# Kernel tuning notes

Hardware: AMD Instinct MI355X
Metric: run time of the kernel (lower is better)

Reference implementation:

```python
import jax, jax.numpy as jnp
import numpy as np

N = 100000   # num_nodes
D = 128      # hidden_dim
E = 640000   # num_edges


def setup_inputs() -> dict:
    key = jax.random.key(0)
    k0, k1, k2, k3 = jax.random.split(key, 4)
    node_features = jax.random.normal(k0, (N, D), dtype=jnp.float32) * 0.02
    # GCNConv linear weights (glorot-style scale), bias initialized to zero
    scale = 1.0 / np.sqrt(D)
    W1 = jax.random.normal(k1, (D, D), dtype=jnp.float32) * scale
    b1 = jnp.zeros((D,), dtype=jnp.float32)
    W2 = jax.random.normal(k2, (D, D), dtype=jnp.float32) * scale
    b2 = jnp.zeros((D,), dtype=jnp.float32)
    edge_index = jax.random.randint(k3, (2, E), 0, N, dtype=jnp.int32)
    return {"node_features": node_features, "W1": W1, "b1": b1,
            "W2": W2, "b2": b2, "edge_index": edge_index}


def gcn_layer(x, W, b, row, col):
    # PyG GCNConv: linear (no bias) -> symmetric norm deg^-1/2 -> scatter-add -> +bias
    x = x @ W.T                                   # [N, D]
    ones = jnp.ones(row.shape, dtype=x.dtype)
    deg = jax.ops.segment_sum(ones, col, num_segments=N)   # in-degree incl. self-loops
    dis = jnp.where(deg > 0, jax.lax.rsqrt(deg), 0.0)       # deg_inv_sqrt, inf -> 0
    norm = dis[row] * dis[col]                    # [E_tot]
    msgs = norm[:, None] * x[row]                 # gather + scale, [E_tot, D]
    out = jax.ops.segment_sum(msgs, col, num_segments=N)    # scatter-aggregate
    return out + b


def reference(node_features, W1, b1, W2, b2, edge_index):
    # add self-loops once (GCNConv does this per call; same result since graph is static)
    loops = jnp.arange(N, dtype=edge_index.dtype)
    row = jnp.concatenate([edge_index[0], loops])
    col = jnp.concatenate([edge_index[1], loops])
    x = jax.nn.relu(gcn_layer(node_features, W1, b1, row, col))
    x = jax.nn.relu(gcn_layer(x, W2, b2, row, col))
    return x
```

## Files before the change

kernel.cpp:

```cpp
#include <hip/hip_runtime.h>

#define DD 128

typedef short bf16x8 __attribute__((ext_vector_type(8)));
typedef float f32x4 __attribute__((ext_vector_type(4)));

__device__ __forceinline__ unsigned short f2bf(float f) {
    unsigned int u = __builtin_bit_cast(unsigned int, f);
    u += 0x7fffu + ((u >> 16) & 1u);
    return (unsigned short)(u >> 16);
}
__device__ __forceinline__ float bflo(unsigned int u) { return __builtin_bit_cast(float, u << 16); }
__device__ __forceinline__ float bfhi(unsigned int u) { return __builtin_bit_cast(float, u & 0xffff0000u); }

__global__ __launch_bounds__(512) void k_count(const int* __restrict__ col,
                                               int* __restrict__ cnt, int E) {
    int e = blockIdx.x * 512 + threadIdx.x;
    if (e < E) atomicAdd(&cnt[col[e]], 1);
}

__global__ __launch_bounds__(256) void k_part(const int* __restrict__ cnt,
                                              int* __restrict__ part, int n) {
    __shared__ int s[256];
    int t = threadIdx.x;
    int i = blockIdx.x * 256 + t;
    s[t] = (i < n) ? cnt[i] : 0;
    __syncthreads();
    for (int off = 128; off > 0; off >>= 1) {
        if (t < off) s[t] += s[t + off];
        __syncthreads();
    }
    if (t == 0) part[blockIdx.x] = s[0];
}

__global__ __launch_bounds__(1024) void k_scanpart(int* __restrict__ part, int nblk) {
    __shared__ int s[1024];
    int t = threadIdx.x;
    int v = (t < nblk) ? part[t] : 0;
    s[t] = v;
    __syncthreads();
    for (int off = 1; off < 1024; off <<= 1) {
        int u = (t >= off) ? s[t - off] : 0;
        __syncthreads();
        s[t] += u;
        __syncthreads();
    }
    if (t < nblk) part[t] = s[t] - v;
}

__global__ __launch_bounds__(256) void k_apply(const int* __restrict__ cnt,
                                               const int* __restrict__ part,
                                               int* __restrict__ rowptr,
                                               int* __restrict__ cursor,
                                               float* __restrict__ dis, int n) {
    __shared__ int s[256];
    int t = threadIdx.x;
    int i = blockIdx.x * 256 + t;
    int c = (i < n) ? cnt[i] : 0;
    s[t] = c;
    __syncthreads();
    for (int off = 1; off < 256; off <<= 1) {
        int u = (t >= off) ? s[t - off] : 0;
        __syncthreads();
        s[t] += u;
        __syncthreads();
    }
    int base = part[blockIdx.x] + s[t] - c;
    if (i < n) {
        rowptr[i] = base;
        cursor[i] = base;
        dis[i] = rsqrtf((float)c + 1.0f);
        if (i == n - 1) rowptr[n] = base + c;
    }
}

#define TILES 2
template <bool INBF16, bool FUSE_PERM>
__global__ __launch_bounds__(512) void k_gemm_mfma(const void* __restrict__ Xv,
                                                   const float* __restrict__ W,
                                                   unsigned short* __restrict__ Y,
                                                   int nrows, int gemm_blocks,
                                                   const int* __restrict__ erow,
                                                   const int* __restrict__ ecol,
                                                   int* __restrict__ cursor,
                                                   int* __restrict__ srow, int E) {
    __shared__ unsigned short Ws[128 * 128];
    const int t = threadIdx.x;

    if (FUSE_PERM && blockIdx.x >= gemm_blocks) {
        int e = (blockIdx.x - gemm_blocks) * 512 + t;
        if (e < E) {
            int p = atomicAdd(&cursor[ecol[e]], 1);
            srow[p] = erow[e];
        }
        return;
    }

    #pragma unroll
    for (int i = 0; i < 4; ++i) {
        int g  = i * 512 + t;
        int wr = g >> 4, ch = g & 15;
        const float* src = W + wr * 128 + ch * 8;
        float4 f0 = *(const float4*)src;
        float4 f1 = *(const float4*)(src + 4);
        unsigned short u[8] = { f2bf(f0.x), f2bf(f0.y), f2bf(f0.z), f2bf(f0.w),
                                f2bf(f1.x), f2bf(f1.y), f2bf(f1.z), f2bf(f1.w) };
        int dst = wr * 128 + ((ch ^ (wr & 15)) << 3);
        *(uint4*)&Ws[dst] = *(const uint4*)u;
    }
    __syncthreads();

    const int wid  = t >> 6;
    const int lane = t & 63;
    const int lr   = lane & 15;
    const int lk   = lane >> 4;

    #pragma unroll
    for (int tile = 0; tile < TILES; ++tile) {
        const long base = ((long)blockIdx.x * TILES + tile) * 128;
        long arow = base + wid * 16 + lr;
        bool rowok = arow < nrows;
        if (!rowok) arow = nrows - 1;

        f32x4 acc[8] = {};

        #pragma unroll
        for (int kc = 0; kc < 4; ++kc) {
            bf16x8 af;
            if (INBF16) {
                const unsigned short* ap = (const unsigned short*)Xv + arow * 128 + kc * 32 + lk * 8;
                af = *(const bf16x8*)ap;
            } else {
                const float* ap = (const float*)Xv + arow * 128 + kc * 32 + lk * 8;
                float4 a0 = *(const float4*)ap;
                float4 a1 = *(const float4*)(ap + 4);
                af[0] = (short)f2bf(a0.x); af[1] = (short)f2bf(a0.y);
                af[2] = (short)f2bf(a0.z); af[3] = (short)f2bf(a0.w);
                af[4] = (short)f2bf(a1.x); af[5] = (short)f2bf(a1.y);
                af[6] = (short)f2bf(a1.z); af[7] = (short)f2bf(a1.w);
            }
            #pragma unroll
            for (int jt = 0; jt < 8; ++jt) {
                int j  = jt * 16 + lr;
                int ch = (kc * 4 + lk) ^ lr;
                const bf16x8* bp = (const bf16x8*)&Ws[j * 128 + (ch << 3)];
                acc[jt] = __builtin_amdgcn_mfma_f32_16x16x32_bf16(*bp, af, acc[jt], 0, 0, 0);
            }
        }

        if (rowok) {
            unsigned short* yp = Y + arow * 128 + lk * 4;
            #pragma unroll
            for (int jt = 0; jt < 8; ++jt) {
                unsigned int d0 = (unsigned int)f2bf(acc[jt][0]) | ((unsigned int)f2bf(acc[jt][1]) << 16);
                unsigned int d1 = (unsigned int)f2bf(acc[jt][2]) | ((unsigned int)f2bf(acc[jt][3]) << 16);
                uint2 u; u.x = d0; u.y = d1;
                *(uint2*)(yp + jt * 16) = u;
            }
        }
    }
}

__device__ __forceinline__ void fma8(float* acc, float nm, uint4 q) {
    acc[0] += nm * bflo(q.x); acc[1] += nm * bfhi(q.x);
    acc[2] += nm * bflo(q.y); acc[3] += nm * bfhi(q.y);
    acc[4] += nm * bflo(q.z); acc[5] += nm * bfhi(q.z);
    acc[6] += nm * bflo(q.w); acc[7] += nm * bfhi(q.w);
}

template <bool OUTBF16>
__global__ __launch_bounds__(256) void k_agg(const int* __restrict__ rowptr,
                                             const int* __restrict__ srow,
                                             const float* __restrict__ dis,
                                             const unsigned short* __restrict__ xw,
                                             const float* __restrict__ b,
                                             void* __restrict__ outv, int n) {
    int v = blockIdx.x * 16 + (threadIdx.x >> 4);
    if (v >= n) return;
    int c = (threadIdx.x & 15) * 8;

    float dv = dis[v], s = dv * dv;
    float acc[8] = {};
    fma8(acc, s, *(const uint4*)(xw + (long)v * 128 + c));

    int e0 = rowptr[v], e1 = rowptr[v + 1];
    int e = e0;
    for (; e + 4 <= e1; e += 4) {
        int   r1 = srow[e],     r2 = srow[e + 1];
        int   r3 = srow[e + 2], r4 = srow[e + 3];
        float n1 = dis[r1] * dv, n2 = dis[r2] * dv;
        float n3 = dis[r3] * dv, n4 = dis[r4] * dv;
        uint4 q1 = *(const uint4*)(xw + (long)r1 * 128 + c);
        uint4 q2 = *(const uint4*)(xw + (long)r2 * 128 + c);
        uint4 q3 = *(const uint4*)(xw + (long)r3 * 128 + c);
        uint4 q4 = *(const uint4*)(xw + (long)r4 * 128 + c);
        fma8(acc, n1, q1);
        fma8(acc, n2, q2);
        fma8(acc, n3, q3);
        fma8(acc, n4, q4);
    }
    for (; e < e1; ++e) {
        int   r1 = srow[e];
        float n1 = dis[r1] * dv;
        fma8(acc, n1, *(const uint4*)(xw + (long)r1 * 128 + c));
    }

    float4 b0 = *(const float4*)(b + c);
    float4 b1 = *(const float4*)(b + c + 4);
    float o[8];
    o[0] = fmaxf(acc[0] + b0.x, 0.0f); o[1] = fmaxf(acc[1] + b0.y, 0.0f);
    o[2] = fmaxf(acc[2] + b0.z, 0.0f); o[3] = fmaxf(acc[3] + b0.w, 0.0f);
    o[4] = fmaxf(acc[4] + b1.x, 0.0f); o[5] = fmaxf(acc[5] + b1.y, 0.0f);
    o[6] = fmaxf(acc[6] + b1.z, 0.0f); o[7] = fmaxf(acc[7] + b1.w, 0.0f);

    if (OUTBF16) {
        unsigned int pk[4];
        pk[0] = (unsigned int)f2bf(o[0]) | ((unsigned int)f2bf(o[1]) << 16);
        pk[1] = (unsigned int)f2bf(o[2]) | ((unsigned int)f2bf(o[3]) << 16);
        pk[2] = (unsigned int)f2bf(o[4]) | ((unsigned int)f2bf(o[5]) << 16);
        pk[3] = (unsigned int)f2bf(o[6]) | ((unsigned int)f2bf(o[7]) << 16);
        *(uint4*)((unsigned short*)outv + (long)v * 128 + c) = *(const uint4*)pk;
    } else {
        float* op = (float*)outv + (long)v * 128 + c;
        *(float4*)op       = make_float4(o[0], o[1], o[2], o[3]);
        *(float4*)(op + 4) = make_float4(o[4], o[5], o[6], o[7]);
    }
}

extern "C" void kernel_launch(void* const* d_in, const int* in_sizes, int n_in,
                              void* d_out, int out_size, void* d_ws, size_t ws_size,
                              hipStream_t stream) {
    const float* X  = (const float*)d_in[0];
    const float* W1 = (const float*)d_in[1];
    const float* b1 = (const float*)d_in[2];
    const float* W2 = (const float*)d_in[3];
    const float* b2 = (const float*)d_in[4];
    const int*   ei = (const int*)d_in[5];
    const int N = in_sizes[0] / DD;
    const int E = in_sizes[5] / 2;
    const int* row = ei;
    const int* col = ei + E;

    char* p = (char*)d_ws;
    auto carve = [&](size_t bytes) { char* q = p; p += (bytes + 255) & ~(size_t)255; return q; };
    int*            cnt    = (int*)           carve((size_t)N * 4);
    int*            rowptr = (int*)           carve((size_t)(N + 1) * 4);
    int*            cursor = (int*)           carve((size_t)N * 4);
    int*            part   = (int*)           carve(1024 * 4);
    int*            srow   = (int*)           carve((size_t)E * 4);
    float*          dis    = (float*)         carve((size_t)N * 4);
    unsigned short* xw     = (unsigned short*)carve((size_t)N * DD * 2);
    unsigned short* h1     = (unsigned short*)d_out;

    const int NBLK = (N + 255) / 256;
    const int gemm_grid  = (N + 128 * TILES - 1) / (128 * TILES);
    const int edge_grid  = (E + 511) / 512;
    const int agg_grid   = (N + 15) / 16;

    hipMemsetAsync(cnt, 0, (size_t)N * 4, stream);
    k_count<<<edge_grid, 512, 0, stream>>>(col, cnt, E);
    k_part<<<NBLK, 256, 0, stream>>>(cnt, part, N);
    k_scanpart<<<1, 1024, 0, stream>>>(part, NBLK);
    k_apply<<<NBLK, 256, 0, stream>>>(cnt, part, rowptr, cursor, dis, N);

    k_gemm_mfma<false, true><<<gemm_grid + edge_grid, 512, 0, stream>>>(
        X, W1, xw, N, gemm_grid, row, col, cursor, srow, E);

    k_agg<true><<<agg_grid, 256, 0, stream>>>(rowptr, srow, dis, xw, b1, h1, N);

    k_gemm_mfma<true, false><<<gemm_grid, 512, 0, stream>>>(
        h1, W2, xw, N, gemm_grid, nullptr, nullptr, nullptr, nullptr, 0);
    k_agg<false><<<agg_grid, 256, 0, stream>>>(rowptr, srow, dis, xw, b2, d_out, N);
}
```

Baseline: 183.6 us.

## Fuse layer-1 aggregation with layer-2 GEMM through shared memory

Measured after the change: 194.1 us. +5.7%, slower.

```diff
diff --git a/kernel.cpp b/kernel.cpp
--- a/kernel.cpp
+++ b/kernel.cpp
@@ -74,9 +74,8 @@
     }
 }
 
-#define TILES 2
-template <bool INBF16, bool FUSE_PERM>
-__global__ __launch_bounds__(512) void k_gemm_mfma(const void* __restrict__ Xv,
+template <bool FUSE_PERM>
+__global__ __launch_bounds__(512) void k_gemm_mfma(const float* __restrict__ Xv,
                                                    const float* __restrict__ W,
                                                    unsigned short* __restrict__ Y,
                                                    int nrows, int gemm_blocks,
@@ -114,49 +113,41 @@
     const int lane = t & 63;
     const int lr   = lane & 15;
     const int lk   = lane >> 4;
-
-    #pragma unroll
-    for (int tile = 0; tile < TILES; ++tile) {
-        const long base = ((long)blockIdx.x * TILES + tile) * 128;
-        long arow = base + wid * 16 + lr;
-        bool rowok = arow < nrows;
-        if (!rowok) arow = nrows - 1;
-
-        f32x4 acc[8] = {};
-
+    const long base = (long)blockIdx.x * 128;
+
+    long arow = base + wid * 16 + lr;
+    bool rowok = arow < nrows;
+    if (!rowok) arow = nrows - 1;
+
+    f32x4 acc[8] = {};
+
+    #pragma unroll
+    for (int kc = 0; kc < 4; ++kc) {
+        const float* ap = Xv + arow * 128 + kc * 32 + lk * 8;
+        float4 a0 = *(const float4*)ap;
+        float4 a1 = *(const float4*)(ap + 4);
+        bf16x8 af;
+        af[0] = (short)f2bf(a0.x); af[1] = (short)f2bf(a0.y);
+        af[2] = (short)f2bf(a0.z); af[3] = (short)f2bf(a0.w);
+        af[4] = (short)f2bf(a1.x); af[5] = (short)f2bf(a1.y);
+        af[6] = (short)f2bf(a1.z); af[7] = (short)f2bf(a1.w);
         #pragma unroll
-        for (int kc = 0; kc < 4; ++kc) {
-            bf16x8 af;
-            if (INBF16) {
-                const unsigned short* ap = (const unsigned short*)Xv + arow * 128 + kc * 32 + lk * 8;
-                af = *(const bf16x8*)ap;
-            } else {
-                const float* ap = (const float*)Xv + arow * 128 + kc * 32 + lk * 8;
-                float4 a0 = *(const float4*)ap;
-                float4 a1 = *(const float4*)(ap + 4);
-                af[0] = (short)f2bf(a0.x); af[1] = (short)f2bf(a0.y);
-                af[2] = (short)f2bf(a0.z); af[3] = (short)f2bf(a0.w);
-                af[4] = (short)f2bf(a1.x); af[5] = (short)f2bf(a1.y);
-                af[6] = (short)f2bf(a1.z); af[7] = (short)f2bf(a1.w);
-            }
-            #pragma unroll
-            for (int jt = 0; jt < 8; ++jt) {
-                int j  = jt * 16 + lr;
-                int ch = (kc * 4 + lk) ^ lr;
-                const bf16x8* bp = (const bf16x8*)&Ws[j * 128 + (ch << 3)];
-                acc[jt] = __builtin_amdgcn_mfma_f32_16x16x32_bf16(*bp, af, acc[jt], 0, 0, 0);
-            }
-        }
-
-        if (rowok) {
-            unsigned short* yp = Y + arow * 128 + lk * 4;
-            #pragma unroll
-            for (int jt = 0; jt < 8; ++jt) {
-                unsigned int d0 = (unsigned int)f2bf(acc[jt][0]) | ((unsigned int)f2bf(acc[jt][1]) << 16);
-                unsigned int d1 = (unsigned int)f2bf(acc[jt][2]) | ((unsigned int)f2bf(acc[jt][3]) << 16);
-                uint2 u; u.x = d0; u.y = d1;
-                *(uint2*)(yp + jt * 16) = u;
-            }
+        for (int jt = 0; jt < 8; ++jt) {
+            int j  = jt * 16 + lr;
+            int ch = (kc * 4 + lk) ^ lr;
+            const bf16x8* bp = (const bf16x8*)&Ws[j * 128 + (ch << 3)];
+            acc[jt] = __builtin_amdgcn_mfma_f32_16x16x32_bf16(*bp, af, acc[jt], 0, 0, 0);
+        }
+    }
+
+    if (rowok) {
+        unsigned short* yp = Y + arow * 128 + lk * 4;
+        #pragma unroll
+        for (int jt = 0; jt < 8; ++jt) {
+            unsigned int d0 = (unsigned int)f2bf(acc[jt][0]) | ((unsigned int)f2bf(acc[jt][1]) << 16);
+            unsigned int d1 = (unsigned int)f2bf(acc[jt][2]) | ((unsigned int)f2bf(acc[jt][3]) << 16);
+            uint2 u; u.x = d0; u.y = d1;
+            *(uint2*)(yp + jt * 16) = u;
         }
     }
 }
@@ -168,20 +159,15 @@
     acc[6] += nm * bflo(q.w); acc[7] += nm * bfhi(q.w);
 }
 
-template <bool OUTBF16>
-__global__ __launch_bounds__(256) void k_agg(const int* __restrict__ rowptr,
-                                             const int* __restrict__ srow,
-                                             const float* __restrict__ dis,
-                                             const unsigned short* __restrict__ xw,
-                                             const float* __restrict__ b,
-                                             void* __restrict__ outv, int n) {
-    int v = blockIdx.x * 16 + (threadIdx.x >> 4);
-    if (v >= n) return;
-    int c = (threadIdx.x & 15) * 8;
-
+__device__ __forceinline__ void agg_node(const int* __restrict__ rowptr,
+                                         const int* __restrict__ srow,
+                                         const float* __restrict__ dis,
+                                         const unsigned short* __restrict__ xw,
+                                         const float* __restrict__ b,
+                                         long v, int c, float* o) {
     float dv = dis[v], s = dv * dv;
     float acc[8] = {};
-    fma8(acc, s, *(const uint4*)(xw + (long)v * 128 + c));
+    fma8(acc, s, *(const uint4*)(xw + v * 128 + c));
 
     int e0 = rowptr[v], e1 = rowptr[v + 1];
     int e = e0;
@@ -194,10 +180,8 @@
         uint4 q2 = *(const uint4*)(xw + (long)r2 * 128 + c);
         uint4 q3 = *(const uint4*)(xw + (long)r3 * 128 + c);
         uint4 q4 = *(const uint4*)(xw + (long)r4 * 128 + c);
-        fma8(acc, n1, q1);
-        fma8(acc, n2, q2);
-        fma8(acc, n3, q3);
-        fma8(acc, n4, q4);
+        fma8(acc, n1, q1); fma8(acc, n2, q2);
+        fma8(acc, n3, q3); fma8(acc, n4, q4);
     }
     for (; e < e1; ++e) {
         int   r1 = srow[e];
@@ -207,24 +191,102 @@
 
     float4 b0 = *(const float4*)(b + c);
     float4 b1 = *(const float4*)(b + c + 4);
-    float o[8];
     o[0] = fmaxf(acc[0] + b0.x, 0.0f); o[1] = fmaxf(acc[1] + b0.y, 0.0f);
     o[2] = fmaxf(acc[2] + b0.z, 0.0f); o[3] = fmaxf(acc[3] + b0.w, 0.0f);
     o[4] = fmaxf(acc[4] + b1.x, 0.0f); o[5] = fmaxf(acc[5] + b1.y, 0.0f);
     o[6] = fmaxf(acc[6] + b1.z, 0.0f); o[7] = fmaxf(acc[7] + b1.w, 0.0f);
-
-    if (OUTBF16) {
+}
+
+__global__ __launch_bounds__(512) void k_agg_gemm(const int* __restrict__ rowptr,
+                                                  const int* __restrict__ srow,
+                                                  const float* __restrict__ dis,
+                                                  const unsigned short* __restrict__ xw,
+                                                  const float* __restrict__ b1,
+                                                  const float* __restrict__ W2,
+                                                  unsigned short* __restrict__ Y,
+                                                  int n) {
+    __shared__ unsigned short Ws[128 * 128];
+    __shared__ unsigned short Hs[128 * 128];
+    const int t = threadIdx.x;
+
+    #pragma unroll
+    for (int i = 0; i < 4; ++i) {
+        int g  = i * 512 + t;
+        int wr = g >> 4, ch = g & 15;
+        const float* src = W2 + wr * 128 + ch * 8;
+        float4 f0 = *(const float4*)src;
+        float4 f1 = *(const float4*)(src + 4);
+        unsigned short u[8] = { f2bf(f0.x), f2bf(f0.y), f2bf(f0.z), f2bf(f0.w),
+                                f2bf(f1.x), f2bf(f1.y), f2bf(f1.z), f2bf(f1.w) };
+        int dst = wr * 128 + ((ch ^ (wr & 15)) << 3);
+        *(uint4*)&Ws[dst] = *(const uint4*)u;
+    }
+
+    const long nb = (long)blockIdx.x * 128;
+    const int c  = (t & 15) * 8;
+    #pragma unroll
+    for (int pass = 0; pass < 4; ++pass) {
+        int  lrow = pass * 32 + (t >> 4);
+        long v    = nb + lrow;
+        float o[8] = {};
+        if (v < n) agg_node(rowptr, srow, dis, xw, b1, v, c, o);
         unsigned int pk[4];
         pk[0] = (unsigned int)f2bf(o[0]) | ((unsigned int)f2bf(o[1]) << 16);
         pk[1] = (unsigned int)f2bf(o[2]) | ((unsigned int)f2bf(o[3]) << 16);
         pk[2] = (unsigned int)f2bf(o[4]) | ((unsigned int)f2bf(o[5]) << 16);
         pk[3] = (unsigned int)f2bf(o[6]) | ((unsigned int)f2bf(o[7]) << 16);
-        *(uint4*)((unsigned short*)outv + (long)v * 128 + c) = *(const uint4*)pk;
-    } else {
-        float* op = (float*)outv + (long)v * 128 + c;
-        *(float4*)op       = make_float4(o[0], o[1], o[2], o[3]);
-        *(float4*)(op + 4) = make_float4(o[4], o[5], o[6], o[7]);
-    }
+        int ch = (t & 15) ^ (lrow & 15);
+        *(uint4*)&Hs[lrow * 128 + (ch << 3)] = *(const uint4*)pk;
+    }
+    __syncthreads();
+
+    const int wid  = t >> 6;
+    const int lane = t & 63;
+    const int lr   = lane & 15;
+    const int lk   = lane >> 4;
+    const int wrow = wid * 16 + lr;
+
+    f32x4 acc[8] = {};
+    #pragma unroll
+    for (int kc = 0; kc < 4; ++kc) {
+        int ach = (kc * 4 + lk) ^ (wrow & 15);
+        bf16x8 af = *(const bf16x8*)&Hs[wrow * 128 + (ach << 3)];
+        #pragma unroll
+        for (int jt = 0; jt < 8; ++jt) {
+            int j  = jt * 16 + lr;
+            int ch = (kc * 4 + lk) ^ lr;
+            const bf16x8* bp = (const bf16x8*)&Ws[j * 128 + (ch << 3)];
+            acc[jt] = __builtin_amdgcn_mfma_f32_16x16x32_bf16(*bp, af, acc[jt], 0, 0, 0);
+        }
+    }
+
+    long grow = nb + wrow;
+    if (grow < n) {
+        unsigned short* yp = Y + grow * 128 + lk * 4;
+        #pragma unroll
+        for (int jt = 0; jt < 8; ++jt) {
+            unsigned int d0 = (unsigned int)f2bf(acc[jt][0]) | ((unsigned int)f2bf(acc[jt][1]) << 16);
+            unsigned int d1 = (unsigned int)f2bf(acc[jt][2]) | ((unsigned int)f2bf(acc[jt][3]) << 16);
+            uint2 u; u.x = d0; u.y = d1;
+            *(uint2*)(yp + jt * 16) = u;
+        }
+    }
+}
+
+__global__ __launch_bounds__(256) void k_agg_out(const int* __restrict__ rowptr,
+                                                 const int* __restrict__ srow,
+                                                 const float* __restrict__ dis,
+                                                 const unsigned short* __restrict__ xw,
+                                                 const float* __restrict__ b,
+                                                 float* __restrict__ out, int n) {
+    long v = blockIdx.x * 16 + (threadIdx.x >> 4);
+    if (v >= n) return;
+    int c = (threadIdx.x & 15) * 8;
+    float o[8];
+    agg_node(rowptr, srow, dis, xw, b, v, c, o);
+    float* op = out + v * 128 + c;
+    *(float4*)op       = make_float4(o[0], o[1], o[2], o[3]);
+    *(float4*)(op + 4) = make_float4(o[4], o[5], o[6], o[7]);
 }
 
 extern "C" void kernel_launch(void* const* d_in, const int* in_sizes, int n_in,
@@ -250,12 +312,12 @@
     int*            srow   = (int*)           carve((size_t)E * 4);
     float*          dis    = (float*)         carve((size_t)N * 4);
     unsigned short* xw     = (unsigned short*)carve((size_t)N * DD * 2);
-    unsigned short* h1     = (unsigned short*)d_out;
+    unsigned short* xw2    = (unsigned short*)carve((size_t)N * DD * 2);
 
     const int NBLK = (N + 255) / 256;
-    const int gemm_grid  = (N + 128 * TILES - 1) / (128 * TILES);
-    const int edge_grid  = (E + 511) / 512;
-    const int agg_grid   = (N + 15) / 16;
+    const int gemm_grid = (N + 127) / 128;
+    const int edge_grid = (E + 511) / 512;
+    const int aggo_grid = (N + 15) / 16;
 
     hipMemsetAsync(cnt, 0, (size_t)N * 4, stream);
     k_count<<<edge_grid, 512, 0, stream>>>(col, cnt, E);
@@ -263,12 +325,10 @@
     k_scanpart<<<1, 1024, 0, stream>>>(part, NBLK);
     k_apply<<<NBLK, 256, 0, stream>>>(cnt, part, rowptr, cursor, dis, N);
 
-    k_gemm_mfma<false, true><<<gemm_grid + edge_grid, 512, 0, stream>>>(
+    k_gemm_mfma<true><<<gemm_grid + edge_grid, 512, 0, stream>>>(
         X, W1, xw, N, gemm_grid, row, col, cursor, srow, E);
 
-    k_agg<true><<<agg_grid, 256, 0, stream>>>(rowptr, srow, dis, xw, b1, h1, N);
-
-    k_gemm_mfma<true, false><<<gemm_grid, 512, 0, stream>>>(
-        h1, W2, xw, N, gemm_grid, nullptr, nullptr, nullptr, nullptr, 0);
-    k_agg<false><<<agg_grid, 256, 0, stream>>>(rowptr, srow, dis, xw, b2, d_out, N);
-}
+    k_agg_gemm<<<gemm_grid, 512, 0, stream>>>(rowptr, srow, dis, xw, b1, W2, xw2, N);
+
+    k_agg_out<<<aggo_grid, 256, 0, stream>>>(rowptr, srow, dis, xw2, b2, (float*)d_out, N);
+}
```
